# Kernel tuning notes

Measured on AMD Instinct MI355X. Metric: run time of the kernel, lower is better.

## Reference

```python
import jax, jax.numpy as jnp
import numpy as np

EPS = 1e-6


def setup_inputs() -> dict:
    key = jax.random.key(0)
    kx, kw = jax.random.split(key)
    B, C, N = 8, 256, 2048
    x = jax.random.normal(kx, (B, C, N), dtype=jnp.float32)
    # nn.Linear(dim*2, 2, bias=False): weight shape [2, 2*C]
    W = jax.random.normal(kw, (2, 2 * C), dtype=jnp.float32) * (1.0 / np.sqrt(2 * C))
    return {"x": x, "W": W}


def reference(x, W):
    B, C, N = x.shape
    # cosine similarity matrix [B, N, N]
    sim = jnp.einsum('bcn,bcm->bnm', x, x)
    # torch: sqrt(sum(x^2 + 1e-6, dim=1)) -> eps added per-channel before sum
    norms = jnp.sqrt(jnp.sum(x * x + EPS, axis=1))            # [B, N]
    io_abs = sim / (norms[:, :, None] * norms[:, None, :])    # [B, N, N]
    # zero the diagonal (fill_diagonal_(0)) before argmax
    io_abs = io_abs * (1.0 - jnp.eye(N, dtype=io_abs.dtype))
    idx = jnp.argmax(io_abs, axis=2)                          # [B, N] nearest-neighbor per token
    # gather retrieved features: f_re[b, :, n] = x[b, :, idx[b, n]]
    f_re = jnp.take_along_axis(x, idx[:, None, :], axis=2)    # [B, C, N]
    # gated fusion
    fus = jnp.concatenate([x, f_re], axis=1).transpose(0, 2, 1)  # [B, N, 2C]
    w = jax.nn.softmax(fus @ W.T, axis=-1)                    # [B, N, 2]
    w = w.transpose(0, 2, 1)                                  # [B, 2, N]
    out = x * w[:, 0:1, :] + f_re * w[:, 1:2, :]
    return (out, f_re)
```

## Files before the change

### kernel.cpp

```cpp
#include <hip/hip_runtime.h>
#include <hip/hip_bf16.h>
#include <math.h>

constexpr int B_ = 8;
constexpr int C_ = 256;
constexpr int N_ = 2048;
constexpr int CN_ = C_ * N_;
constexpr int TOT_ = B_ * C_ * N_;
constexpr int BN_ = B_ * N_;
constexpr int NTILES = 16;
constexpr int NPAIRS = 136;
constexpr float EPSC = 256.0f * 1e-6f;

typedef __attribute__((ext_vector_type(8))) short bf16x8;
typedef __attribute__((ext_vector_type(4))) float f32x4;
typedef __attribute__((ext_vector_type(2))) unsigned int u32x2;

__device__ __forceinline__ void g2l16(const void* g, void* l) {
    __builtin_amdgcn_global_load_lds(
        (const __attribute__((address_space(1))) void*)g,
        (__attribute__((address_space(3))) void*)l, 16, 0, 0);
}

__device__ __forceinline__ unsigned short bits(__hip_bfloat16 h) {
    union { __hip_bfloat16 b; unsigned short u; } cv;
    cv.b = h;
    return cv.u;
}

__device__ __forceinline__ float b2f(short s) {
    union { float f; unsigned u; } cv;
    cv.u = ((unsigned)(unsigned short)s) << 16;
    return cv.f;
}

__device__ __forceinline__ unsigned long long packkey(float v, int m) {
    const unsigned b = __float_as_uint(v);
    const unsigned u = (b & 0x80000000u) ? ~b : (b | 0x80000000u);
    return ((unsigned long long)u << 32) | (unsigned)(2047 - m);
}

__device__ __forceinline__ unsigned packpair(float a, float b) {
    return ((unsigned)bits(__float2bfloat16(b)) << 16) | bits(__float2bfloat16(a));
}

__device__ __forceinline__ float rnormsum(const float* __restrict__ normp, int idx) {
    return 1.0f / sqrtf(normp[idx] + normp[BN_ + idx] + normp[2 * BN_ + idx] +
                        normp[3 * BN_ + idx] + EPSC);
}

__global__ __launch_bounds__(256) void convert_kernel(const float* __restrict__ x,
                                                      __hip_bfloat16* __restrict__ hiT,
                                                      __hip_bfloat16* __restrict__ loT,
                                                      float* __restrict__ normp,
                                                      int* __restrict__ rcnt) {
    const int blk = blockIdx.x;
    const int batch = blk & 7;
    const int nt = (blk >> 3) & 31;
    const int ctile = blk >> 8;
    const int n0 = nt << 6, c0 = ctile << 6;
    const int t = threadIdx.x;

    if (blk == 0 && t == 0) rcnt[0] = 0;

    __shared__ float tb[64][65];
    __shared__ float red[16][65];

    const int i4 = t & 15;
    const int j = t >> 4;
    const float* xp = x + (size_t)batch * CN_ + (size_t)c0 * N_ + n0;
#pragma unroll
    for (int p = 0; p < 4; ++p) {
        const int cl = j + p * 16;
        const float4 v = *(const float4*)(xp + (size_t)cl * N_ + 4 * i4);
        tb[cl][4 * i4 + 0] = v.x;
        tb[cl][4 * i4 + 1] = v.y;
        tb[cl][4 * i4 + 2] = v.z;
        tb[cl][4 * i4 + 3] = v.w;
    }
    __syncthreads();

    const int cq = t & 15;
    const int nb = t >> 4;
    const int c = cq << 2;
#pragma unroll
    for (int r = 0; r < 4; ++r) {
        const int n = nb + r * 16;
        const float v0 = tb[c][n], v1 = tb[c + 1][n];
        const float v2 = tb[c + 2][n], v3 = tb[c + 3][n];
        const __hip_bfloat16 h0 = __float2bfloat16(v0);
        const __hip_bfloat16 h1 = __float2bfloat16(v1);
        const __hip_bfloat16 h2 = __float2bfloat16(v2);
        const __hip_bfloat16 h3 = __float2bfloat16(v3);
        const float g0 = v0 - __bfloat162float(h0);
        const float g1 = v1 - __bfloat162float(h1);
        const float g2 = v2 - __bfloat162float(h2);
        const float g3 = v3 - __bfloat162float(h3);
        red[cq][n] = v0 * v0 + v1 * v1 + v2 * v2 + v3 * v3;
        const size_t o = ((size_t)batch * N_ + n0 + n) * C_ + c0 + c;
        u32x2 hp, lp;
        hp[0] = ((unsigned)bits(h1) << 16) | bits(h0);
        hp[1] = ((unsigned)bits(h3) << 16) | bits(h2);
        lp[0] = packpair(g0, g1);
        lp[1] = packpair(g2, g3);
        ((u32x2*)hiT)[o >> 2] = hp;
        ((u32x2*)loT)[o >> 2] = lp;
        __syncthreads();
    }
    if (t < 64) {
        float s = 0.f;
#pragma unroll
        for (int g = 0; g < 16; ++g) s += red[g][t];
        normp[ctile * BN_ + batch * N_ + n0 + t] = s;
    }
}

__global__ __launch_bounds__(512) void gram_mfma_kernel(
        const __hip_bfloat16* __restrict__ hiT, const __hip_bfloat16* __restrict__ loT,
        const float* __restrict__ normp,
        float* __restrict__ pval, int* __restrict__ pidx, float* __restrict__ pval2) {
    const int blk = blockIdx.x;
    const int batch = blk & 7;
    int p = blk >> 3;
    int bn = 0;
    while (p >= NTILES - bn) { p -= NTILES - bn; ++bn; }
    const int bm = bn + p;
    const bool diag = (bn == bm);
    const int n0 = bn << 7, m0 = bm << 7;

    __shared__ short As0[128 * 64];
    __shared__ short As1[128 * 64];
    __shared__ short Bs0[128 * 64];
    __shared__ short Bs1[128 * 64];
    short* ov = &As0[0];
    float (*rv1)[4] = (float(*)[4])(ov + 0);
    int (*ri1)[4] = (int(*)[4])(ov + 1024);
    float (*rv2)[4] = (float(*)[4])(ov + 2048);
    float (*cv1)[2] = (float(*)[2])(ov + 3072);
    int (*ci1)[2] = (int(*)[2])(ov + 3584);
    float (*cv2)[2] = (float(*)[2])(ov + 4096);
    float* rnA = (float*)(ov + 4608);

    const int tid = threadIdx.x;
    const int l = tid & 63, w = tid >> 6;
    const int lm = l & 15, q = l >> 4;
    const int x7 = lm & 7;
    const int wn = (w >> 2) << 6;
    const int wm = (w & 3) << 5;

    const size_t bbase = (size_t)batch * CN_;
    const short* gA[2];
    const short* gB[2];
    int ldsoff[2];
#pragma unroll
    for (int pp = 0; pp < 2; ++pp) {
        const int slot = tid + pp * 512;
        const int r = slot >> 3, sidx = slot & 7;
        const int sw = sidx ^ (r & 7);
        const short* base = (const short*)((sw < 4) ? hiT : loT);
        gA[pp] = base + bbase + (size_t)(n0 + r) * C_ + (sw & 3) * 8;
        gB[pp] = base + bbase + (size_t)(m0 + r) * C_ + (sw & 3) * 8;
        ldsoff[pp] = slot * 8;
    }
    int aoff[8], boff[4];
#pragma unroll
    for (int rt = 0; rt < 4; ++rt) {
        const int ra = wn + rt * 16 + lm;
        aoff[rt * 2] = ra * 64 + ((q ^ x7) * 8);
        aoff[rt * 2 + 1] = ra * 64 + (((4 | q) ^ x7) * 8);
    }
#pragma unroll
    for (int ct = 0; ct < 2; ++ct) {
        const int rb = wm + ct * 16 + lm;
        boff[ct * 2] = rb * 64 + ((q ^ x7) * 8);
        boff[ct * 2 + 1] = rb * 64 + (((4 | q) ^ x7) * 8);
    }

    f32x4 acc[4][2];
#pragma unroll
    for (int rt = 0; rt < 4; ++rt)
#pragma unroll
        for (int ct = 0; ct < 2; ++ct) acc[rt][ct] = (f32x4){0.f, 0.f, 0.f, 0.f};

#pragma unroll
    for (int pp = 0; pp < 2; ++pp) {
        g2l16(gA[pp], As0 + ldsoff[pp]);
        g2l16(gB[pp], Bs0 + ldsoff[pp]);
    }
    __syncthreads();

#pragma unroll
    for (int kt = 0; kt < 8; ++kt) {
        short* Ac = (kt & 1) ? As1 : As0;
        short* Bc = (kt & 1) ? Bs1 : Bs0;
        if (kt < 7) {
            short* An = (kt & 1) ? As0 : As1;
            short* Bn = (kt & 1) ? Bs0 : Bs1;
#pragma unroll
            for (int pp = 0; pp < 2; ++pp) {
                g2l16(gA[pp] + (kt + 1) * 32, An + ldsoff[pp]);
                g2l16(gB[pp] + (kt + 1) * 32, Bn + ldsoff[pp]);
            }
        }
        bf16x8 ah[4], al[4], bh[2], bl[2];
#pragma unroll
        for (int rt = 0; rt < 4; ++rt) {
            ah[rt] = *(const bf16x8*)(Ac + aoff[rt * 2]);
            al[rt] = *(const bf16x8*)(Ac + aoff[rt * 2 + 1]);
        }
#pragma unroll
        for (int ct = 0; ct < 2; ++ct) {
            bh[ct] = *(const bf16x8*)(Bc + boff[ct * 2]);
            bl[ct] = *(const bf16x8*)(Bc + boff[ct * 2 + 1]);
        }
        __builtin_amdgcn_s_setprio(1);
#pragma unroll
        for (int rt = 0; rt < 4; ++rt)
#pragma unroll
            for (int ct = 0; ct < 2; ++ct) {
                acc[rt][ct] = __builtin_amdgcn_mfma_f32_16x16x32_bf16(
                    ah[rt], bh[ct], acc[rt][ct], 0, 0, 0);
                acc[rt][ct] = __builtin_amdgcn_mfma_f32_16x16x32_bf16(
                    ah[rt], bl[ct], acc[rt][ct], 0, 0, 0);
                acc[rt][ct] = __builtin_amdgcn_mfma_f32_16x16x32_bf16(
                    al[rt], bh[ct], acc[rt][ct], 0, 0, 0);
            }
        __builtin_amdgcn_s_setprio(0);
        __syncthreads();
    }

    if (tid < 128) rnA[tid] = rnormsum(normp, batch * N_ + n0 + tid);

    float rnm[2];
#pragma unroll
    for (int ct = 0; ct < 2; ++ct)
        rnm[ct] = rnormsum(normp, batch * N_ + m0 + wm + ct * 16 + lm);

#pragma unroll
    for (int rt = 0; rt < 4; ++rt) {
#pragma unroll
        for (int r = 0; r < 4; ++r) {
            const int nrow = n0 + wn + rt * 16 + q * 4 + r;
            float v1 = -3.4e38f, v2 = -3.4e38f;
            int i1 = 0x7fffffff;
#pragma unroll
            for (int ct = 0; ct < 2; ++ct) {
                const int m = m0 + wm + ct * 16 + lm;
                const float v = acc[rt][ct][r] * rnm[ct];
                if (m == nrow) continue;
                if (v > v1) { v2 = v1; v1 = v; i1 = m; }
                else if (v > v2) v2 = v;
            }
#pragma unroll
            for (int d = 1; d < 16; d <<= 1) {
                const float ov1 = __shfl_xor(v1, d, 64);
                const int oi1 = __shfl_xor(i1, d, 64);
                const float ov2 = __shfl_xor(v2, d, 64);
                if (ov1 > v1 || (ov1 == v1 && oi1 < i1)) {
                    v2 = fmaxf(v1, ov2); v1 = ov1; i1 = oi1;
                } else {
                    v2 = fmaxf(v2, ov1);
                }
            }
            if (lm == 0) {
                const int rloc = wn + rt * 16 + q * 4 + r;
                rv1[rloc][w & 3] = v1;
                ri1[rloc][w & 3] = i1;
                rv2[rloc][w & 3] = v2;
            }
        }
    }
    __syncthreads();

    if (!diag) {
        float rnn[4][4];
#pragma unroll
        for (int rt = 0; rt < 4; ++rt)
#pragma unroll
            for (int r = 0; r < 4; ++r) rnn[rt][r] = rnA[wn + rt * 16 + q * 4 + r];
#pragma unroll
        for (int ct = 0; ct < 2; ++ct) {
            float v1 = -3.4e38f, v2 = -3.4e38f;
            int i1 = 0x7fffffff;
#pragma unroll
            for (int rt = 0; rt < 4; ++rt) {
#pragma unroll
                for (int r = 0; r < 4; ++r) {
                    const float v = acc[rt][ct][r] * rnn[rt][r];
                    const int nn = n0 + wn + rt * 16 + q * 4 + r;
                    if (v > v1) { v2 = v1; v1 = v; i1 = nn; }
                    else if (v > v2) v2 = v;
                }
            }
#pragma unroll
            for (int d = 16; d < 64; d <<= 1) {
                const float ov1 = __shfl_xor(v1, d, 64);
                const int oi1 = __shfl_xor(i1, d, 64);
                const float ov2 = __shfl_xor(v2, d, 64);
                if (ov1 > v1 || (ov1 == v1 && oi1 < i1)) {
                    v2 = fmaxf(v1, ov2); v1 = ov1; i1 = oi1;
                } else {
                    v2 = fmaxf(v2, ov1);
                }
            }
            if (q == 0) {
                const int mloc = wm + ct * 16 + lm;
                cv1[mloc][w >> 2] = v1;
                ci1[mloc][w >> 2] = i1;
                cv2[mloc][w >> 2] = v2;
            }
        }
    }
    __syncthreads();

    if (tid < 128) {
        {
            float v1 = rv1[tid][0]; int i1 = ri1[tid][0]; float v2 = rv2[tid][0];
#pragma unroll
            for (int s = 1; s < 4; ++s) {
                const float ov1 = rv1[tid][s]; const int oi1 = ri1[tid][s]; const float ov2 = rv2[tid][s];
                if (ov1 > v1 || (ov1 == v1 && oi1 < i1)) { v2 = fmaxf(v1, ov2); v1 = ov1; i1 = oi1; }
                else v2 = fmaxf(v2, ov1);
            }
            const size_t gi = (size_t)(batch * NTILES + bm) * N_ + n0 + tid;
            pval[gi] = v1; pidx[gi] = i1; pval2[gi] = v2;
        }
        if (!diag) {
            float v1 = cv1[tid][0]; int i1 = ci1[tid][0]; float v2 = cv2[tid][0];
            const float ov1 = cv1[tid][1]; const int oi1 = ci1[tid][1]; const float ov2 = cv2[tid][1];
            if (ov1 > v1 || (ov1 == v1 && oi1 < i1)) { v2 = fmaxf(v1, ov2); v1 = ov1; i1 = oi1; }
            else v2 = fmaxf(v2, ov1);
            const size_t gi = (size_t)(batch * NTILES + bn) * N_ + m0 + tid;
            pval[gi] = v1; pidx[gi] = i1; pval2[gi] = v2;
        }
    }
}

__global__ void combine_kernel(const float* __restrict__ pval, const int* __restrict__ pidx,
                               const float* __restrict__ pval2, int* __restrict__ fidx,
                               int* __restrict__ rcnt, int* __restrict__ ridx,
                               unsigned long long* __restrict__ pbest) {
    const int gt = blockIdx.x * 256 + threadIdx.x;
    const int row = gt >> 2, part = gt & 3;
    const int batch = row >> 11, n = row & 2047;
    float v1 = -3.4e38f, v2 = -3.4e38f;
    int i1 = 0x7fffffff;
    for (int s = part; s < NTILES; s += 4) {
        const size_t gi = (size_t)(batch * NTILES + s) * N_ + n;
        const float ov1 = pval[gi]; const int oi1 = pidx[gi]; const float ov2 = pval2[gi];
        if (ov1 > v1 || (ov1 == v1 && oi1 < i1)) { v2 = fmaxf(v1, ov2); v1 = ov1; i1 = oi1; }
        else v2 = fmaxf(v2, ov1);
    }
#pragma unroll
    for (int d = 1; d < 4; d <<= 1) {
        const float ov1 = __shfl_xor(v1, d, 64);
        const int oi1 = __shfl_xor(i1, d, 64);
        const float ov2 = __shfl_xor(v2, d, 64);
        if (ov1 > v1 || (ov1 == v1 && oi1 < i1)) { v2 = fmaxf(v1, ov2); v1 = ov1; i1 = oi1; }
        else v2 = fmaxf(v2, ov1);
    }
    if (part == 0) {
        fidx[row] = i1;
        if (v1 - v2 < 4e-5f) {
            const int slot = atomicAdd(rcnt, 1);
            ridx[slot] = row;
            pbest[slot] = 0ull;
        }
    }
}

__global__ __launch_bounds__(256) void rescue_kernel(const float* __restrict__ x,
                                                     const float* __restrict__ normp,
                                                     const int* __restrict__ rcnt,
                                                     const int* __restrict__ ridx,
                                                     unsigned long long* __restrict__ pbest) {
    const int cnt = *rcnt;
    const int nwork = cnt << 3;
    const int tid = threadIdx.x;
    __shared__ unsigned long long bk[256];
    for (int wi = blockIdx.x; wi < nwork; wi += gridDim.x) {
        const int rr = wi >> 3, ch = wi & 7;
        const int t = ridx[rr];
        const int batch = t >> 11, n = t & 2047;
        const int m = (ch << 8) + tid;
        const float* xb = x + (size_t)batch * CN_;
        float s0 = 0.f, s1 = 0.f, s2 = 0.f, s3 = 0.f;
        const float* xn = xb + n;
        const float* xm = xb + m;
#pragma unroll 4
        for (int c = 0; c < C_; c += 4) {
            s0 += xn[(size_t)(c + 0) * N_] * xm[(size_t)(c + 0) * N_];
            s1 += xn[(size_t)(c + 1) * N_] * xm[(size_t)(c + 1) * N_];
            s2 += xn[(size_t)(c + 2) * N_] * xm[(size_t)(c + 2) * N_];
            s3 += xn[(size_t)(c + 3) * N_] * xm[(size_t)(c + 3) * N_];
        }
        const float v = ((s0 + s1) + (s2 + s3)) * rnormsum(normp, batch * N_ + m);
        bk[tid] = (m == n) ? 0ull : packkey(v, m);
        __syncthreads();
        for (int sft = 128; sft > 0; sft >>= 1) {
            if (tid < sft) {
                const unsigned long long o = bk[tid + sft];
                if (o > bk[tid]) bk[tid] = o;
            }
            __syncthreads();
        }
        if (tid == 0) atomicMax(&pbest[rr], bk[0]);
        __syncthreads();
    }
}

__global__ __launch_bounds__(512) void finish_kernel(const float* __restrict__ x,
                                                     const __hip_bfloat16* __restrict__ hiT,
                                                     const __hip_bfloat16* __restrict__ loT,
                                                     const float* __restrict__ W,
                                                     const int* __restrict__ fidx,
                                                     const int* __restrict__ rcnt,
                                                     const int* __restrict__ ridx,
                                                     const unsigned long long* __restrict__ pbest,
                                                     float* __restrict__ out) {
    const int batch = blockIdx.x & 7;
    const int nt = blockIdx.x >> 3;
    const int n0 = nt << 4;
    const int t = threadIdx.x;
    const int i = t & 15, cg = t >> 4;

    __shared__ float Wl[1024];
    __shared__ int il[16];
    __shared__ float pl0[32][17], pl1[32][17];
    __shared__ float w0s[16], w1s[16];

    for (int u = t; u < 1024; u += 512) Wl[u] = W[u];
    if (t < 16) il[t] = fidx[batch * N_ + n0 + t];
    __syncthreads();
    {
        const int cnt = *rcnt;
        for (int rr = t; rr < cnt; rr += 512) {
            const int tt = ridx[rr];
            if ((tt >> 11) == batch) {
                const int n = tt & 2047;
                if (n >= n0 && n < n0 + 16) {
                    const unsigned long long k = pbest[rr];
                    il[n - n0] = 2047 - (int)(unsigned)(k & 0xffffffffull);
                }
            }
        }
    }
    __syncthreads();

    const int myrow = il[i];
    const size_t rowb = ((size_t)batch * N_ + myrow) * C_ + cg * 8;

    float fre[8];
    {
        const bf16x8 h = *(const bf16x8*)(hiT + rowb);
        const bf16x8 g = *(const bf16x8*)(loT + rowb);
#pragma unroll
        for (int e = 0; e < 8; ++e) fre[e] = b2f(h[e]) + b2f(g[e]);
    }

    const float* xb = x + (size_t)batch * CN_ + n0 + i;
    float xr[8];
    float l0 = 0.f, l1 = 0.f;
#pragma unroll
    for (int cc = 0; cc < 8; ++cc) {
        const int c = cg * 8 + cc;
        const float xv = xb[(size_t)c * N_];
        xr[cc] = xv;
        l0 += xv * Wl[c] + fre[cc] * Wl[256 + c];
        l1 += xv * Wl[512 + c] + fre[cc] * Wl[768 + c];
    }
    pl0[cg][i] = l0;
    pl1[cg][i] = l1;
    __syncthreads();
    if (t < 16) {
        float L0 = 0.f, L1 = 0.f;
#pragma unroll
        for (int g = 0; g < 32; ++g) { L0 += pl0[g][t]; L1 += pl1[g][t]; }
        const float mx = fmaxf(L0, L1);
        const float e0 = expf(L0 - mx);
        const float e1 = expf(L1 - mx);
        const float inv = 1.0f / (e0 + e1);
        w0s[t] = e0 * inv;
        w1s[t] = e1 * inv;
    }
    __syncthreads();
    const float w0 = w0s[i], w1 = w1s[i];

#pragma unroll
    for (int cc = 0; cc < 8; ++cc) {
        const int c = cg * 8 + cc;
        const size_t off = (size_t)batch * CN_ + (size_t)c * N_ + n0 + i;
        __builtin_nontemporal_store(xr[cc] * w0 + fre[cc] * w1, out + off);
        __builtin_nontemporal_store(fre[cc], out + TOT_ + off);
    }
}

extern "C" void kernel_launch(void* const* d_in, const int* in_sizes, int n_in,
                              void* d_out, int out_size, void* d_ws, size_t ws_size,
                              hipStream_t stream) {
    const float* x = (const float*)d_in[0];
    const float* W = (const float*)d_in[1];
    float* out = (float*)d_out;

    const size_t BF_BYTES = (size_t)TOT_ * 2;
    const size_t NORM_BYTES = (size_t)BN_ * 4;
    const size_t P_BYTES = (size_t)B_ * NTILES * N_ * 4;

    uint8_t* p = (uint8_t*)d_ws;
    __hip_bfloat16* hiT = (__hip_bfloat16*)p; p += BF_BYTES;
    __hip_bfloat16* loT = (__hip_bfloat16*)p; p += BF_BYTES;
    float* normp = (float*)p; p += 4 * NORM_BYTES;
    float* pval = (float*)p; p += P_BYTES;
    int* pidx = (int*)p; p += P_BYTES;
    float* pval2 = (float*)p; p += P_BYTES;
    int* fidx = (int*)p; p += NORM_BYTES;
    int* rcnt = (int*)p; p += 256;
    int* ridx = (int*)p; p += NORM_BYTES;
    unsigned long long* pbest = (unsigned long long*)p; p += (size_t)BN_ * 8;

    convert_kernel<<<1024, 256, 0, stream>>>(x, hiT, loT, normp, rcnt);
    gram_mfma_kernel<<<B_ * NPAIRS, 512, 0, stream>>>(hiT, loT, normp, pval, pidx, pval2);
    combine_kernel<<<256, 256, 0, stream>>>(pval, pidx, pval2, fidx, rcnt, ridx, pbest);
    rescue_kernel<<<2048, 256, 0, stream>>>(x, normp, rcnt, ridx, pbest);
    finish_kernel<<<1024, 512, 0, stream>>>(x, hiT, loT, W, fidx, rcnt, ridx, pbest, out);
}
```

Before: 167.3 us.

## Replace double-buffered K loop with single-buffer 64-wide K stages

The gram MFMA kernel no longer double-buffers 32-wide K slices. It now loads 64-wide K chunks of the hi and lo bf16 planes into one shared buffer per operand, using a new swizzled layout, and runs four stages instead of eight. This halves the number of barrier-separated iterations and makes each global-to-LDS transfer larger. In exchange, loads no longer overlap with MFMA compute, because each stage waits for its load before computing and needs a second barrier before the buffer is overwritten.

```diff
diff --git a/kernel.cpp b/kernel.cpp
--- a/kernel.cpp
+++ b/kernel.cpp
@@ -128,11 +128,9 @@
     const bool diag = (bn == bm);
     const int n0 = bn << 7, m0 = bm << 7;
 
-    __shared__ short As0[128 * 64];
-    __shared__ short As1[128 * 64];
-    __shared__ short Bs0[128 * 64];
-    __shared__ short Bs1[128 * 64];
-    short* ov = &As0[0];
+    __shared__ short As[128 * 128];
+    __shared__ short Bs[128 * 128];
+    short* ov = &As[0];
     float (*rv1)[4] = (float(*)[4])(ov + 0);
     int (*ri1)[4] = (int(*)[4])(ov + 1024);
     float (*rv2)[4] = (float(*)[4])(ov + 2048);
@@ -149,31 +147,31 @@
     const int wm = (w & 3) << 5;
 
     const size_t bbase = (size_t)batch * CN_;
-    const short* gA[2];
-    const short* gB[2];
-    int ldsoff[2];
-#pragma unroll
-    for (int pp = 0; pp < 2; ++pp) {
+    const short* gA[4];
+    const short* gB[4];
+    int ldsoff[4];
+#pragma unroll
+    for (int pp = 0; pp < 4; ++pp) {
         const int slot = tid + pp * 512;
-        const int r = slot >> 3, sidx = slot & 7;
-        const int sw = sidx ^ (r & 7);
-        const short* base = (const short*)((sw < 4) ? hiT : loT);
-        gA[pp] = base + bbase + (size_t)(n0 + r) * C_ + (sw & 3) * 8;
-        gB[pp] = base + bbase + (size_t)(m0 + r) * C_ + (sw & 3) * 8;
+        const int r = slot >> 4, sidx = slot & 15;
+        const int kg = (sidx & 7) ^ (r & 7);
+        const short* base = (const short*)((sidx < 8) ? hiT : loT);
+        gA[pp] = base + bbase + (size_t)(n0 + r) * C_ + kg * 8;
+        gB[pp] = base + bbase + (size_t)(m0 + r) * C_ + kg * 8;
         ldsoff[pp] = slot * 8;
     }
-    int aoff[8], boff[4];
+    int aoffh[4], aoffl[4], boffh[2], boffl[2];
 #pragma unroll
     for (int rt = 0; rt < 4; ++rt) {
         const int ra = wn + rt * 16 + lm;
-        aoff[rt * 2] = ra * 64 + ((q ^ x7) * 8);
-        aoff[rt * 2 + 1] = ra * 64 + (((4 | q) ^ x7) * 8);
+        aoffh[rt] = ra * 128 + ((q ^ x7) * 8);
+        aoffl[rt] = ra * 128 + 64 + ((q ^ x7) * 8);
     }
 #pragma unroll
     for (int ct = 0; ct < 2; ++ct) {
         const int rb = wm + ct * 16 + lm;
-        boff[ct * 2] = rb * 64 + ((q ^ x7) * 8);
-        boff[ct * 2 + 1] = rb * 64 + (((4 | q) ^ x7) * 8);
+        boffh[ct] = rb * 128 + ((q ^ x7) * 8);
+        boffl[ct] = rb * 128 + 64 + ((q ^ x7) * 8);
     }
 
     f32x4 acc[4][2];
@@ -183,51 +181,44 @@
         for (int ct = 0; ct < 2; ++ct) acc[rt][ct] = (f32x4){0.f, 0.f, 0.f, 0.f};
 
 #pragma unroll
-    for (int pp = 0; pp < 2; ++pp) {
-        g2l16(gA[pp], As0 + ldsoff[pp]);
-        g2l16(gB[pp], Bs0 + ldsoff[pp]);
-    }
-    __syncthreads();
-
-#pragma unroll
-    for (int kt = 0; kt < 8; ++kt) {
-        short* Ac = (kt & 1) ? As1 : As0;
-        short* Bc = (kt & 1) ? Bs1 : Bs0;
-        if (kt < 7) {
-            short* An = (kt & 1) ? As0 : As1;
-            short* Bn = (kt & 1) ? Bs0 : Bs1;
-#pragma unroll
-            for (int pp = 0; pp < 2; ++pp) {
-                g2l16(gA[pp] + (kt + 1) * 32, An + ldsoff[pp]);
-                g2l16(gB[pp] + (kt + 1) * 32, Bn + ldsoff[pp]);
-            }
-        }
-        bf16x8 ah[4], al[4], bh[2], bl[2];
-#pragma unroll
-        for (int rt = 0; rt < 4; ++rt) {
-            ah[rt] = *(const bf16x8*)(Ac + aoff[rt * 2]);
-            al[rt] = *(const bf16x8*)(Ac + aoff[rt * 2 + 1]);
-        }
-#pragma unroll
-        for (int ct = 0; ct < 2; ++ct) {
-            bh[ct] = *(const bf16x8*)(Bc + boff[ct * 2]);
-            bl[ct] = *(const bf16x8*)(Bc + boff[ct * 2 + 1]);
-        }
-        __builtin_amdgcn_s_setprio(1);
-#pragma unroll
-        for (int rt = 0; rt < 4; ++rt)
+    for (int kt = 0; kt < 4; ++kt) {
+        __syncthreads();
+#pragma unroll
+        for (int pp = 0; pp < 4; ++pp) {
+            g2l16(gA[pp] + kt * 64, As + ldsoff[pp]);
+            g2l16(gB[pp] + kt * 64, Bs + ldsoff[pp]);
+        }
+        __syncthreads();
+#pragma unroll
+        for (int kq = 0; kq < 2; ++kq) {
+            const int kx = kq << 5;
+            bf16x8 ah[4], al[4], bh[2], bl[2];
+#pragma unroll
+            for (int rt = 0; rt < 4; ++rt) {
+                ah[rt] = *(const bf16x8*)(As + (aoffh[rt] ^ kx));
+                al[rt] = *(const bf16x8*)(As + (aoffl[rt] ^ kx));
+            }
 #pragma unroll
             for (int ct = 0; ct < 2; ++ct) {
-                acc[rt][ct] = __builtin_amdgcn_mfma_f32_16x16x32_bf16(
-                    ah[rt], bh[ct], acc[rt][ct], 0, 0, 0);
-                acc[rt][ct] = __builtin_amdgcn_mfma_f32_16x16x32_bf16(
-                    ah[rt], bl[ct], acc[rt][ct], 0, 0, 0);
-                acc[rt][ct] = __builtin_amdgcn_mfma_f32_16x16x32_bf16(
-                    al[rt], bh[ct], acc[rt][ct], 0, 0, 0);
-            }
-        __builtin_amdgcn_s_setprio(0);
-        __syncthreads();
-    }
+                bh[ct] = *(const bf16x8*)(Bs + (boffh[ct] ^ kx));
+                bl[ct] = *(const bf16x8*)(Bs + (boffl[ct] ^ kx));
+            }
+            __builtin_amdgcn_s_setprio(1);
+#pragma unroll
+            for (int rt = 0; rt < 4; ++rt)
+#pragma unroll
+                for (int ct = 0; ct < 2; ++ct) {
+                    acc[rt][ct] = __builtin_amdgcn_mfma_f32_16x16x32_bf16(
+                        ah[rt], bh[ct], acc[rt][ct], 0, 0, 0);
+                    acc[rt][ct] = __builtin_amdgcn_mfma_f32_16x16x32_bf16(
+                        ah[rt], bl[ct], acc[rt][ct], 0, 0, 0);
+                    acc[rt][ct] = __builtin_amdgcn_mfma_f32_16x16x32_bf16(
+                        al[rt], bh[ct], acc[rt][ct], 0, 0, 0);
+                }
+            __builtin_amdgcn_s_setprio(0);
+        }
+    }
+    __syncthreads();
 
     if (tid < 128) rnA[tid] = rnormsum(normp, batch * N_ + n0 + tid);
 
```

Measured after the change: 167.0 us. No clear change (-0.2%).
